# Optimization experiments

Measured on AMD Instinct MI355X. Metric: run time of the kernel, lower is better.

The kernel has to match this reference:

```python
import jax, jax.numpy as jnp
import numpy as np

N_NODES = 50000
N_EDGES = 500000
HIDDEN = 64
NUM_BASIS = 32
NUM_SH = 4  # (lmax+1)^2 with lmax=1


def _mlp(x, w1, b1, w2, b2):
    # Linear -> SiLU -> Linear, matching nn.Sequential(Linear, SiLU, Linear)
    return jax.nn.silu(x @ w1 + b1) @ w2 + b2


def setup_inputs() -> dict:
    key = jax.random.key(0)
    ks = jax.random.split(key, 10)
    scale_in = 1.0 / np.sqrt(NUM_BASIS)
    scale_h = 1.0 / np.sqrt(HIDDEN)
    return {
        "scalar": jax.random.normal(ks[0], (N_NODES, HIDDEN), dtype=jnp.float32),
        "vector": jax.random.normal(ks[1], (N_NODES, 3, HIDDEN), dtype=jnp.float32),
        "edge_sh": jax.random.normal(ks[2], (N_EDGES, NUM_SH), dtype=jnp.float32),
        "edge_length": jax.random.uniform(ks[3], (N_EDGES, NUM_BASIS), dtype=jnp.float32),
        "edge_index": jax.random.randint(ks[4], (2, N_EDGES), 0, N_NODES, dtype=jnp.int32),
        "sw1": jax.random.normal(ks[5], (NUM_BASIS, HIDDEN), dtype=jnp.float32) * scale_in,
        "sb1": jnp.zeros((HIDDEN,), dtype=jnp.float32),
        "sw2": jax.random.normal(ks[6], (HIDDEN, HIDDEN), dtype=jnp.float32) * scale_h,
        "sb2": jnp.zeros((HIDDEN,), dtype=jnp.float32),
        "vw1": jax.random.normal(ks[7], (NUM_BASIS, HIDDEN), dtype=jnp.float32) * scale_in,
        "vb1": jnp.zeros((HIDDEN,), dtype=jnp.float32),
        "vw2": jax.random.normal(ks[8], (HIDDEN, HIDDEN), dtype=jnp.float32) * scale_h,
        "vb2": jnp.zeros((HIDDEN,), dtype=jnp.float32),
    }


def reference(scalar, vector, edge_sh, edge_length, edge_index,
              sw1, sb1, sw2, sb2, vw1, vb1, vw2, vb2):
    # edge_sh is accepted (as in the torch forward signature) but unused.
    row, col = edge_index[0], edge_index[1]
    n = scalar.shape[0]

    # Edge-wise MLP weights from radial basis expansion: [E, hidden]
    scalar_weights = _mlp(edge_length, sw1, sb1, sw2, sb2)
    # Gather source-node scalars, weight, scatter-add to destination nodes.
    scalar_msg = scalar[col] * scalar_weights                   # [E, hidden]
    out_scalar = jax.ops.segment_sum(scalar_msg, row, num_segments=n)

    vector_weights = _mlp(edge_length, vw1, vb1, vw2, vb2)      # [E, hidden]
    vector_msg = vector[col] * vector_weights[:, None, :]       # [E, 3, hidden]
    out_vector = jax.ops.segment_sum(vector_msg, row, num_segments=n)

    return out_scalar, out_vector
```

## Files before the change

### kernel.cpp

```cpp
#include <hip/hip_runtime.h>

#define HIDDEN 64
#define NB 32
#define SCAN_BLOCK 1024
#define HSTR 72

typedef __attribute__((ext_vector_type(8))) short bf16x8;
typedef __attribute__((ext_vector_type(4))) float f32x4;

static __device__ __forceinline__ unsigned short f2bf(float x) {
    union { float f; unsigned u; } v; v.f = x;
    unsigned r = v.u + 0x7fffu + ((v.u >> 16) & 1u);
    return (unsigned short)(r >> 16);
}
static __device__ __forceinline__ float bf2f(unsigned short s) {
    union { unsigned u; float f; } v; v.u = ((unsigned)s) << 16;
    return v.f;
}

__global__ __launch_bounds__(256) void featpack_kernel(
    const float* __restrict__ scalar,
    const float* __restrict__ vector,
    ushort4* __restrict__ feat,
    int total)
{
    int i = blockIdx.x * 256 + threadIdx.x;
    if (i >= total) return;
    const int n = i >> 6, l = i & 63;
    const float* vp = vector + (size_t)n * 192 + l;
    ushort4 o;
    o.x = f2bf(scalar[i]);
    o.y = f2bf(vp[0]);
    o.z = f2bf(vp[64]);
    o.w = f2bf(vp[128]);
    feat[i] = o;
}

__global__ __launch_bounds__(SCAN_BLOCK) void scan_pass1(
    const int* __restrict__ counts, int* __restrict__ partial,
    int* __restrict__ blocksums, int N)
{
    __shared__ int tmp[SCAN_BLOCK];
    const int t = threadIdx.x;
    const int gid = blockIdx.x * SCAN_BLOCK + t;
    int v = (gid < N) ? counts[gid] : 0;
    tmp[t] = v;
    __syncthreads();
    for (int off = 1; off < SCAN_BLOCK; off <<= 1) {
        int x = (t >= off) ? tmp[t - off] : 0;
        __syncthreads();
        tmp[t] += x;
        __syncthreads();
    }
    if (gid < N) partial[gid] = tmp[t] - v;
    if (t == SCAN_BLOCK - 1) blocksums[blockIdx.x] = tmp[t];
}

__global__ __launch_bounds__(64) void scan_pass2(int* __restrict__ blocksums, int nb)
{
    const int t = threadIdx.x;
    int v = (t < nb) ? blocksums[t] : 0;
    int s = v;
    #pragma unroll
    for (int off = 1; off < 64; off <<= 1) {
        int x = __shfl_up(s, off, 64);
        if (t >= off) s += x;
    }
    if (t < nb) blocksums[t] = s - v;
}

__global__ __launch_bounds__(SCAN_BLOCK) void scan_pass3(
    const int* __restrict__ partial, const int* __restrict__ blocksums,
    int* __restrict__ offsets, int* __restrict__ cursors, int N, int E)
{
    const int gid = blockIdx.x * SCAN_BLOCK + threadIdx.x;
    if (gid < N) {
        int o = partial[gid] + blocksums[blockIdx.x];
        offsets[gid] = o;
        cursors[gid] = o;
    }
    if (blockIdx.x == 0 && threadIdx.x == 0) offsets[N] = E;
}

__global__ __launch_bounds__(256) void scatter_kernel(
    const int* __restrict__ edge_index, int* __restrict__ cursors,
    int2* __restrict__ pc, int E)
{
    int i = blockIdx.x * 256 + threadIdx.x;
    if (i < E) {
        int pos = atomicAdd(&cursors[edge_index[i]], 1);
        pc[pos] = make_int2(i, edge_index[E + i]);
    }
}

__global__ __launch_bounds__(256) void mlp_mfma_kernel(
    const float* __restrict__ edge_length,
    const int*   __restrict__ edge_index,
    int* __restrict__ counts,
    const float* __restrict__ sw1, const float* __restrict__ sb1,
    const float* __restrict__ sw2, const float* __restrict__ sb2,
    const float* __restrict__ vw1, const float* __restrict__ vb1,
    const float* __restrict__ vw2, const float* __restrict__ vb2,
    unsigned short* __restrict__ W,
    int E, int nchunks)
{
    __shared__ short Hs[4][64 * HSTR];

    const int t    = threadIdx.x;
    const int lane = t & 63;
    const int wid  = t >> 6;
    const int quad = lane >> 4;
    const int l16  = lane & 15;
    short* Hw = Hs[wid];

    const float* w1p[2] = {sw1, vw1};
    const float* b1p[2] = {sb1, vb1};
    const float* w2p[2] = {sw2, vw2};
    const float* b2p[2] = {sb2, vb2};

    bf16x8 w1f[2][4];
    bf16x8 w2f[2][2][4];
    float  b1v[2][4], b2v[2][4];
    #pragma unroll
    for (int m = 0; m < 2; ++m) {
        #pragma unroll
        for (int nt = 0; nt < 4; ++nt) {
            const int col = nt * 16 + l16;
            #pragma unroll
            for (int j = 0; j < 8; ++j)
                w1f[m][nt][j] = (short)f2bf(w1p[m][(quad * 8 + j) * HIDDEN + col]);
            #pragma unroll
            for (int kk = 0; kk < 2; ++kk) {
                #pragma unroll
                for (int j = 0; j < 8; ++j)
                    w2f[m][kk][nt][j] = (short)f2bf(w2p[m][(kk * 32 + quad * 8 + j) * HIDDEN + col]);
            }
            b1v[m][nt] = b1p[m][col];
            b2v[m][nt] = b2p[m][col];
        }
    }

    const int wave_g = blockIdx.x * 4 + wid;
    const int nwaves = gridDim.x * 4;

    for (int c = wave_g; c < nchunks; c += nwaves) {
        const int j0 = c * 64;

        {
            const int e = j0 + lane;
            if (e < E) atomicAdd(&counts[edge_index[e]], 1);
        }

        bf16x8 af[4];
        #pragma unroll
        for (int mt = 0; mt < 4; ++mt) {
            int e = j0 + mt * 16 + l16;
            if (e >= E) e = E - 1;
            const float* r = edge_length + (size_t)e * NB + quad * 8;
            float4 u0 = *(const float4*)r;
            float4 u1 = *(const float4*)(r + 4);
            af[mt][0] = (short)f2bf(u0.x); af[mt][1] = (short)f2bf(u0.y);
            af[mt][2] = (short)f2bf(u0.z); af[mt][3] = (short)f2bf(u0.w);
            af[mt][4] = (short)f2bf(u1.x); af[mt][5] = (short)f2bf(u1.y);
            af[mt][6] = (short)f2bf(u1.z); af[mt][7] = (short)f2bf(u1.w);
        }

        #pragma unroll
        for (int m = 0; m < 2; ++m) {
            #pragma unroll
            for (int mt = 0; mt < 4; ++mt) {
                #pragma unroll
                for (int nt = 0; nt < 4; ++nt) {
                    f32x4 cf = {b1v[m][nt], b1v[m][nt], b1v[m][nt], b1v[m][nt]};
                    cf = __builtin_amdgcn_mfma_f32_16x16x32_bf16(af[mt], w1f[m][nt], cf, 0, 0, 0);
                    #pragma unroll
                    for (int r4 = 0; r4 < 4; ++r4) {
                        float x = cf[r4];
                        x = x / (1.0f + __expf(-x));
                        const int row = mt * 16 + quad * 4 + r4;
                        Hw[row * HSTR + nt * 16 + l16] = (short)f2bf(x);
                    }
                }
            }

            #pragma unroll
            for (int mt = 0; mt < 4; ++mt) {
                const int arow = mt * 16 + l16;
                bf16x8 a0 = *(const bf16x8*)(Hw + arow * HSTR + quad * 8);
                bf16x8 a1 = *(const bf16x8*)(Hw + arow * HSTR + 32 + quad * 8);
                #pragma unroll
                for (int nt = 0; nt < 4; ++nt) {
                    f32x4 cf = {b2v[m][nt], b2v[m][nt], b2v[m][nt], b2v[m][nt]};
                    cf = __builtin_amdgcn_mfma_f32_16x16x32_bf16(a1, w2f[m][1][nt], cf, 0, 0, 0);
                    cf = __builtin_amdgcn_mfma_f32_16x16x32_bf16(a0, w2f[m][0][nt], cf, 0, 0, 0);
                    #pragma unroll
                    for (int r4 = 0; r4 < 4; ++r4) {
                        const int row = mt * 16 + quad * 4 + r4;
                        Hw[row * HSTR + nt * 16 + l16] = (short)f2bf(cf[r4]);
                    }
                }
            }

            #pragma unroll
            for (int i = 0; i < 8; ++i) {
                const int row = i * 8 + (lane >> 3);
                bf16x8 v = *(const bf16x8*)(Hw + row * HSTR + (lane & 7) * 8);
                if (j0 + row < E)
                    *(bf16x8*)(W + (size_t)(j0 + row) * 128 + m * 64 + (lane & 7) * 8) = v;
            }
        }
    }
}

__global__ __launch_bounds__(256) void node_kernel_feat(
    const ushort4* __restrict__ feat,
    const int* __restrict__ offsets,
    const int2* __restrict__ pc,
    const unsigned short* __restrict__ W,
    float* __restrict__ out_scalar,
    float* __restrict__ out_vector,
    int N)
{
    const int lane = threadIdx.x & 63;
    const int wave = blockIdx.x * 4 + (threadIdx.x >> 6);
    const int nw   = gridDim.x * 4;

    for (int n = wave; n < N; n += nw) {
        const int beg = offsets[n];
        const int end = offsets[n + 1];

        float as = 0.0f, a0 = 0.0f, a1 = 0.0f, a2 = 0.0f;
        float ws = 0, wv = 0, s = 0, v0 = 0, v1 = 0, v2 = 0;

        if (beg < end) {
            const int2 p = pc[beg];
            const unsigned short* wp = W + (size_t)p.x * 128;
            ws = bf2f(wp[lane]); wv = bf2f(wp[64 + lane]);
            const ushort4 f = feat[(size_t)p.y * 64 + lane];
            s = bf2f(f.x); v0 = bf2f(f.y); v1 = bf2f(f.z); v2 = bf2f(f.w);
        }

        for (int j = beg; j < end; ++j) {
            const int jn = (j + 1 < end) ? j + 1 : j;
            const int2 p = pc[jn];
            const unsigned short* wp = W + (size_t)p.x * 128;
            const float wsn = bf2f(wp[lane]);
            const float wvn = bf2f(wp[64 + lane]);
            const ushort4 f = feat[(size_t)p.y * 64 + lane];
            const float sn  = bf2f(f.x);
            const float v0n = bf2f(f.y);
            const float v1n = bf2f(f.z);
            const float v2n = bf2f(f.w);

            as = fmaf(s,  ws, as);
            a0 = fmaf(v0, wv, a0);
            a1 = fmaf(v1, wv, a1);
            a2 = fmaf(v2, wv, a2);

            ws = wsn; wv = wvn; s = sn; v0 = v0n; v1 = v1n; v2 = v2n;
        }

        out_scalar[(size_t)n * HIDDEN + lane] = as;
        float* ov = out_vector + (size_t)n * 3 * HIDDEN;
        ov[lane]       = a0;
        ov[64 + lane]  = a1;
        ov[128 + lane] = a2;
    }
}

__global__ __launch_bounds__(256) void node_kernel_f32(
    const float* __restrict__ scalar,
    const float* __restrict__ vector,
    const int* __restrict__ offsets,
    const int2* __restrict__ pc,
    const unsigned short* __restrict__ W,
    float* __restrict__ out_scalar,
    float* __restrict__ out_vector,
    int N)
{
    const int lane = threadIdx.x & 63;
    const int wave = blockIdx.x * 4 + (threadIdx.x >> 6);
    const int nw   = gridDim.x * 4;

    for (int n = wave; n < N; n += nw) {
        const int beg = offsets[n];
        const int end = offsets[n + 1];
        float as = 0.0f, a0 = 0.0f, a1 = 0.0f, a2 = 0.0f;
        for (int j = beg; j < end; ++j) {
            const int2 p = pc[j];
            const unsigned short* wp = W + (size_t)p.x * 128;
            const float w_s = bf2f(wp[lane]);
            const float w_v = bf2f(wp[64 + lane]);
            const float* sp = scalar + (size_t)p.y * HIDDEN;
            const float* vp = vector + (size_t)p.y * 3 * HIDDEN;
            as = fmaf(sp[lane],       w_s, as);
            a0 = fmaf(vp[lane],       w_v, a0);
            a1 = fmaf(vp[64 + lane],  w_v, a1);
            a2 = fmaf(vp[128 + lane], w_v, a2);
        }
        out_scalar[(size_t)n * HIDDEN + lane] = as;
        float* ov = out_vector + (size_t)n * 3 * HIDDEN;
        ov[lane]       = a0;
        ov[64 + lane]  = a1;
        ov[128 + lane] = a2;
    }
}

extern "C" void kernel_launch(void* const* d_in, const int* in_sizes, int n_in,
                              void* d_out, int out_size, void* d_ws, size_t ws_size,
                              hipStream_t stream) {
    const float* scalar      = (const float*)d_in[0];
    const float* vector      = (const float*)d_in[1];
    const float* edge_length = (const float*)d_in[3];
    const int*   edge_index  = (const int*)d_in[4];
    const float* sw1 = (const float*)d_in[5];
    const float* sb1 = (const float*)d_in[6];
    const float* sw2 = (const float*)d_in[7];
    const float* sb2 = (const float*)d_in[8];
    const float* vw1 = (const float*)d_in[9];
    const float* vb1 = (const float*)d_in[10];
    const float* vw2 = (const float*)d_in[11];
    const float* vb2 = (const float*)d_in[12];

    const int N = in_sizes[0] / HIDDEN;
    const int E = in_sizes[4] / 2;

    float* out_scalar = (float*)d_out;
    float* out_vector = (float*)d_out + (size_t)N * HIDDEN;

    size_t off = 0;
    unsigned short* W = (unsigned short*)d_ws;
    off += (size_t)E * 128 * 2;
    int2* pc = (int2*)((char*)d_ws + off);
    off += (size_t)E * 8;
    int* ib = (int*)((char*)d_ws + off);
    int* counts    = ib;
    int* partial   = ib + N;
    int* offsets   = ib + 2 * N;
    int* cursors   = ib + 3 * N + 1;
    int* blocksums = ib + 4 * N + 1;
    off += ((size_t)4 * N + 1 + 64) * 4;
    off = (off + 15) & ~(size_t)15;
    ushort4* feat = (ushort4*)((char*)d_ws + off);
    const bool use_feat = (off + (size_t)N * 64 * 8) <= ws_size;

    hipMemsetAsync(counts, 0, (size_t)N * sizeof(int), stream);

    const int egrid = (E + 255) / 256;

    if (use_feat) {
        const int total = N * 64;
        featpack_kernel<<<(total + 255) / 256, 256, 0, stream>>>(
            scalar, vector, feat, total);
    }

    const int nchunks = (E + 63) / 64;
    mlp_mfma_kernel<<<512, 256, 0, stream>>>(
        edge_length, edge_index, counts,
        sw1, sb1, sw2, sb2, vw1, vb1, vw2, vb2,
        W, E, nchunks);

    const int nb = (N + SCAN_BLOCK - 1) / SCAN_BLOCK;
    scan_pass1<<<nb, SCAN_BLOCK, 0, stream>>>(counts, partial, blocksums, N);
    scan_pass2<<<1, 64, 0, stream>>>(blocksums, nb);
    scan_pass3<<<nb, SCAN_BLOCK, 0, stream>>>(partial, blocksums, offsets, cursors, N, E);
    scatter_kernel<<<egrid, 256, 0, stream>>>(edge_index, cursors, pc, E);

    const int ngrid = (N + 3) / 4;
    if (use_feat) {
        node_kernel_feat<<<ngrid, 256, 0, stream>>>(
            feat, offsets, pc, W, out_scalar, out_vector, N);
    } else {
        node_kernel_f32<<<ngrid, 256, 0, stream>>>(
            scalar, vector, offsets, pc, W, out_scalar, out_vector, N);
    }
}
```

Before: 334.1 us.

## Write edge weights in CSR order and move degree counting into featpack

```diff
diff --git a/kernel.cpp b/kernel.cpp
--- a/kernel.cpp
+++ b/kernel.cpp
@@ -21,11 +21,14 @@
 __global__ __launch_bounds__(256) void featpack_kernel(
     const float* __restrict__ scalar,
     const float* __restrict__ vector,
+    const int*   __restrict__ edge_index,
+    int* __restrict__ counts,
     ushort4* __restrict__ feat,
-    int total)
+    int total, int E, int do_feat)
 {
     int i = blockIdx.x * 256 + threadIdx.x;
-    if (i >= total) return;
+    if (i < E) atomicAdd(&counts[edge_index[i]], 1);
+    if (!do_feat || i >= total) return;
     const int n = i >> 6, l = i & 63;
     const float* vp = vector + (size_t)n * 192 + l;
     ushort4 o;
@@ -84,19 +87,19 @@
 
 __global__ __launch_bounds__(256) void scatter_kernel(
     const int* __restrict__ edge_index, int* __restrict__ cursors,
-    int2* __restrict__ pc, int E)
+    int* __restrict__ cols, int* __restrict__ posArr, int E)
 {
     int i = blockIdx.x * 256 + threadIdx.x;
     if (i < E) {
-        int pos = atomicAdd(&cursors[edge_index[i]], 1);
-        pc[pos] = make_int2(i, edge_index[E + i]);
-    }
-}
-
-__global__ __launch_bounds__(256) void mlp_mfma_kernel(
+        int p = atomicAdd(&cursors[edge_index[i]], 1);
+        cols[p] = edge_index[E + i];
+        posArr[i] = p;
+    }
+}
+
+__global__ __launch_bounds__(256, 4) void mlp_mfma_kernel(
     const float* __restrict__ edge_length,
-    const int*   __restrict__ edge_index,
-    int* __restrict__ counts,
+    const int*   __restrict__ posArr,
     const float* __restrict__ sw1, const float* __restrict__ sb1,
     const float* __restrict__ sw2, const float* __restrict__ sb2,
     const float* __restrict__ vw1, const float* __restrict__ vb1,
@@ -145,11 +148,6 @@
 
     for (int c = wave_g; c < nchunks; c += nwaves) {
         const int j0 = c * 64;
-
-        {
-            const int e = j0 + lane;
-            if (e < E) atomicAdd(&counts[edge_index[e]], 1);
-        }
 
         bf16x8 af[4];
         #pragma unroll
@@ -176,7 +174,7 @@
                     #pragma unroll
                     for (int r4 = 0; r4 < 4; ++r4) {
                         float x = cf[r4];
-                        x = x / (1.0f + __expf(-x));
+                        x = x * __builtin_amdgcn_rcpf(1.0f + __expf(-x));
                         const int row = mt * 16 + quad * 4 + r4;
                         Hw[row * HSTR + nt * 16 + l16] = (short)f2bf(x);
                     }
@@ -205,8 +203,11 @@
             for (int i = 0; i < 8; ++i) {
                 const int row = i * 8 + (lane >> 3);
                 bf16x8 v = *(const bf16x8*)(Hw + row * HSTR + (lane & 7) * 8);
-                if (j0 + row < E)
-                    *(bf16x8*)(W + (size_t)(j0 + row) * 128 + m * 64 + (lane & 7) * 8) = v;
+                const int e = j0 + row;
+                if (e < E) {
+                    const int p = posArr[e];
+                    *(bf16x8*)(W + (size_t)p * 128 + m * 64 + (lane & 7) * 8) = v;
+                }
             }
         }
     }
@@ -215,7 +216,7 @@
 __global__ __launch_bounds__(256) void node_kernel_feat(
     const ushort4* __restrict__ feat,
     const int* __restrict__ offsets,
-    const int2* __restrict__ pc,
+    const int* __restrict__ cols,
     const unsigned short* __restrict__ W,
     float* __restrict__ out_scalar,
     float* __restrict__ out_vector,
@@ -233,20 +234,18 @@
         float ws = 0, wv = 0, s = 0, v0 = 0, v1 = 0, v2 = 0;
 
         if (beg < end) {
-            const int2 p = pc[beg];
-            const unsigned short* wp = W + (size_t)p.x * 128;
+            const unsigned short* wp = W + (size_t)beg * 128;
             ws = bf2f(wp[lane]); wv = bf2f(wp[64 + lane]);
-            const ushort4 f = feat[(size_t)p.y * 64 + lane];
+            const ushort4 f = feat[(size_t)cols[beg] * 64 + lane];
             s = bf2f(f.x); v0 = bf2f(f.y); v1 = bf2f(f.z); v2 = bf2f(f.w);
         }
 
         for (int j = beg; j < end; ++j) {
             const int jn = (j + 1 < end) ? j + 1 : j;
-            const int2 p = pc[jn];
-            const unsigned short* wp = W + (size_t)p.x * 128;
+            const unsigned short* wp = W + (size_t)jn * 128;
             const float wsn = bf2f(wp[lane]);
             const float wvn = bf2f(wp[64 + lane]);
-            const ushort4 f = feat[(size_t)p.y * 64 + lane];
+            const ushort4 f = feat[(size_t)cols[jn] * 64 + lane];
             const float sn  = bf2f(f.x);
             const float v0n = bf2f(f.y);
             const float v1n = bf2f(f.z);
@@ -272,7 +271,7 @@
     const float* __restrict__ scalar,
     const float* __restrict__ vector,
     const int* __restrict__ offsets,
-    const int2* __restrict__ pc,
+    const int* __restrict__ cols,
     const unsigned short* __restrict__ W,
     float* __restrict__ out_scalar,
     float* __restrict__ out_vector,
@@ -287,12 +286,12 @@
         const int end = offsets[n + 1];
         float as = 0.0f, a0 = 0.0f, a1 = 0.0f, a2 = 0.0f;
         for (int j = beg; j < end; ++j) {
-            const int2 p = pc[j];
-            const unsigned short* wp = W + (size_t)p.x * 128;
+            const unsigned short* wp = W + (size_t)j * 128;
             const float w_s = bf2f(wp[lane]);
             const float w_v = bf2f(wp[64 + lane]);
-            const float* sp = scalar + (size_t)p.y * HIDDEN;
-            const float* vp = vector + (size_t)p.y * 3 * HIDDEN;
+            const int c = cols[j];
+            const float* sp = scalar + (size_t)c * HIDDEN;
+            const float* vp = vector + (size_t)c * 3 * HIDDEN;
             as = fmaf(sp[lane],       w_s, as);
             a0 = fmaf(vp[lane],       w_v, a0);
             a1 = fmaf(vp[64 + lane],  w_v, a1);
@@ -331,8 +330,10 @@
     size_t off = 0;
     unsigned short* W = (unsigned short*)d_ws;
     off += (size_t)E * 128 * 2;
-    int2* pc = (int2*)((char*)d_ws + off);
-    off += (size_t)E * 8;
+    int* cols = (int*)((char*)d_ws + off);
+    off += (size_t)E * 4;
+    int* posArr = (int*)((char*)d_ws + off);
+    off += (size_t)E * 4;
     int* ib = (int*)((char*)d_ws + off);
     int* counts    = ib;
     int* partial   = ib + N;
@@ -348,30 +349,31 @@
 
     const int egrid = (E + 255) / 256;
 
-    if (use_feat) {
+    {
         const int total = N * 64;
-        featpack_kernel<<<(total + 255) / 256, 256, 0, stream>>>(
-            scalar, vector, feat, total);
-    }
-
-    const int nchunks = (E + 63) / 64;
-    mlp_mfma_kernel<<<512, 256, 0, stream>>>(
-        edge_length, edge_index, counts,
-        sw1, sb1, sw2, sb2, vw1, vb1, vw2, vb2,
-        W, E, nchunks);
+        int cover = total > E ? total : E;
+        featpack_kernel<<<(cover + 255) / 256, 256, 0, stream>>>(
+            scalar, vector, edge_index, counts, feat, total, E, use_feat ? 1 : 0);
+    }
 
     const int nb = (N + SCAN_BLOCK - 1) / SCAN_BLOCK;
     scan_pass1<<<nb, SCAN_BLOCK, 0, stream>>>(counts, partial, blocksums, N);
     scan_pass2<<<1, 64, 0, stream>>>(blocksums, nb);
     scan_pass3<<<nb, SCAN_BLOCK, 0, stream>>>(partial, blocksums, offsets, cursors, N, E);
-    scatter_kernel<<<egrid, 256, 0, stream>>>(edge_index, cursors, pc, E);
+    scatter_kernel<<<egrid, 256, 0, stream>>>(edge_index, cursors, cols, posArr, E);
+
+    const int nchunks = (E + 63) / 64;
+    mlp_mfma_kernel<<<1024, 256, 0, stream>>>(
+        edge_length, posArr,
+        sw1, sb1, sw2, sb2, vw1, vb1, vw2, vb2,
+        W, E, nchunks);
 
     const int ngrid = (N + 3) / 4;
     if (use_feat) {
         node_kernel_feat<<<ngrid, 256, 0, stream>>>(
-            feat, offsets, pc, W, out_scalar, out_vector, N);
+            feat, offsets, cols, W, out_scalar, out_vector, N);
     } else {
         node_kernel_f32<<<ngrid, 256, 0, stream>>>(
-            scalar, vector, offsets, pc, W, out_scalar, out_vector, N);
-    }
-}
+            scalar, vector, offsets, cols, W, out_scalar, out_vector, N);
+    }
+}
```

Result: slower. 420.1 us (+25.7%).
